# Optimization experiments

Measured on AMD Instinct MI355X. Metric: run time of the kernel, lower is better.

Reference implementation:

```python
import jax, jax.numpy as jnp
import numpy as np

B, T, DIN, H, DOUT = 256, 512, 128, 256, 64
LEAK = 0.01


def setup_inputs() -> dict:
    key = jax.random.key(0)
    k0, k1, k2, k3, k4, k5, k6 = jax.random.split(key, 7)
    inputs = jax.random.normal(k0, (B, T, DIN), dtype=jnp.float32)
    # original uses torch.rand(...) * sqrt(dim) for initial states
    x0 = jax.random.uniform(k1, (B, DOUT), dtype=jnp.float32) * (DOUT ** 0.5)
    h0 = jax.random.uniform(k2, (B, H), dtype=jnp.float32) * (H ** 0.5)
    # nn.Linear default init scale ~ 1/sqrt(fan_in)
    s1 = (DIN + H) ** -0.5
    s2 = H ** -0.5
    W_ih = jax.random.uniform(k3, (H, DIN + H), dtype=jnp.float32, minval=-s1, maxval=s1)
    b_ih = jax.random.uniform(k4, (H,), dtype=jnp.float32, minval=-s1, maxval=s1)
    W_ho = jax.random.uniform(k5, (DOUT, H), dtype=jnp.float32, minval=-s2, maxval=s2)
    b_ho = jax.random.uniform(k6, (DOUT,), dtype=jnp.float32, minval=-s2, maxval=s2)
    return {"inputs": inputs, "x0": x0, "h0": h0,
            "W_ih": W_ih, "b_ih": b_ih, "W_ho": W_ho, "b_ho": b_ho}


def reference(inputs, x0, h0, W_ih, b_ih, W_ho, b_ho):
    # inputs: [B, T, DIN]; scan over time with hidden state resident.
    def step(h, u_t):  # h: [B,H], u_t: [B,DIN]
        comb = jnp.concatenate([u_t, h], axis=1)           # [B, DIN+H]
        pre = comb @ W_ih.T + b_ih                          # [B, H]
        h_new = jnp.where(pre >= 0, pre, LEAK * pre)        # LeakyReLU(0.01)
        x_t = h_new @ W_ho.T + b_ho                         # [B, DOUT]
        return h_new, (x_t, h_new)

    u_seq = jnp.swapaxes(inputs, 0, 1)                      # [T, B, DIN]
    _, (xs, hs) = jax.lax.scan(step, h0, u_seq)
    # prepend initial states -> [B, T+1, *]
    x = jnp.concatenate([x0[:, None, :], jnp.swapaxes(xs, 0, 1)], axis=1)
    h = jnp.concatenate([h0[:, None, :], jnp.swapaxes(hs, 0, 1)], axis=1)
    return x, h
```

## Files before the change

kernel.cpp:

```cpp
#include <hip/hip_runtime.h>

#define BB 256
#define TT 512
#define DIN 128
#define HH 256
#define DOUT 64
#define XROWS ((long)BB * 513)
#define X_ELEMS ((long)BB * 513 * DOUT)

typedef short bf16x8 __attribute__((ext_vector_type(8)));
typedef float f32x4 __attribute__((ext_vector_type(4)));
typedef _Float16 half2_t __attribute__((ext_vector_type(2)));
typedef _Float16 half8_t __attribute__((ext_vector_type(8)));

static __device__ inline short f2bf(float f) {
    unsigned u = __float_as_uint(f);
    unsigned r = (u + 0x7FFFu + ((u >> 16) & 1u)) >> 16;
    return (short)r;
}

static __device__ inline float fdot2f(half2_t a, half2_t b, float c) {
#if __has_builtin(__builtin_amdgcn_fdot2)
    return __builtin_amdgcn_fdot2(a, b, c, false);
#else
    return c + (float)a[0] * (float)b[0] + (float)a[1] * (float)b[1];
#endif
}

__global__ __launch_bounds__(256) void gemm_u(
        const float* __restrict__ inp, const float* __restrict__ W_ih,
        const float* __restrict__ b_ih, float* __restrict__ out_h) {
    __shared__ __align__(16) short lA[64 * 40];
    __shared__ __align__(16) short lB[64 * 40];
    const int tid = threadIdx.x;
    const int wave = tid >> 6, lane = tid & 63;
    const int quad = lane >> 4, l16 = lane & 15;
    const int m0 = blockIdx.x * 64;
    const int n0 = blockIdx.y * 64;
    const int sm = tid >> 2, skg = tid & 3;
    const int sn = tid & 63, bkg = tid >> 6;

    f32x4 acc[4];
#pragma unroll
    for (int i = 0; i < 4; i++) acc[i] = (f32x4){0.f, 0.f, 0.f, 0.f};

#pragma unroll
    for (int k0 = 0; k0 < DIN; k0 += 32) {
        const float4* ap = (const float4*)(inp + (long)(m0 + sm) * DIN + k0 + skg * 8);
        float4 a0 = ap[0], a1 = ap[1];
        const float4* bp = (const float4*)(W_ih + (long)(n0 + sn) * 384 + k0 + bkg * 8);
        float4 b0 = bp[0], b1 = bp[1];
        __syncthreads();
        bf16x8 av, bv;
        av[0] = f2bf(a0.x); av[1] = f2bf(a0.y); av[2] = f2bf(a0.z); av[3] = f2bf(a0.w);
        av[4] = f2bf(a1.x); av[5] = f2bf(a1.y); av[6] = f2bf(a1.z); av[7] = f2bf(a1.w);
        bv[0] = f2bf(b0.x); bv[1] = f2bf(b0.y); bv[2] = f2bf(b0.z); bv[3] = f2bf(b0.w);
        bv[4] = f2bf(b1.x); bv[5] = f2bf(b1.y); bv[6] = f2bf(b1.z); bv[7] = f2bf(b1.w);
        *(bf16x8*)&lA[sm * 40 + skg * 8] = av;
        *(bf16x8*)&lB[sn * 40 + bkg * 8] = bv;
        __syncthreads();
        bf16x8 af = *(const bf16x8*)&lA[(wave * 16 + l16) * 40 + quad * 8];
#pragma unroll
        for (int nt = 0; nt < 4; nt++) {
            bf16x8 bf = *(const bf16x8*)&lB[(nt * 16 + l16) * 40 + quad * 8];
            acc[nt] = __builtin_amdgcn_mfma_f32_16x16x32_bf16(af, bf, acc[nt], 0, 0, 0);
        }
    }
#pragma unroll
    for (int nt = 0; nt < 4; nt++) {
#pragma unroll
        for (int r = 0; r < 4; r++) {
            int m = m0 + wave * 16 + quad * 4 + r;
            int col = n0 + nt * 16 + l16;
            long orow = (long)(m >> 9) * 513 + (m & 511) + 1;
            out_h[orow * HH + col] = acc[nt][r] + b_ih[col];
        }
    }
}

__global__ __launch_bounds__(512) void rnn_seq(
        const float* __restrict__ x0, const float* __restrict__ h0,
        const float* __restrict__ W_ih,
        float* __restrict__ out_x, float* __restrict__ out_h) {
    __shared__ __align__(16) _Float16 hsh[HH];
    __shared__ float part[HH];
    const int b = blockIdx.x;
    const int tid = threadIdx.x;
    const int wave = tid >> 6, lane = tid & 63;
    const int jg = wave & 3, kh = wave >> 2;
    const int j = jg * 64 + lane;
    const int kbase = kh * 128;

    half2_t w[64];
    const float* wr = W_ih + (long)j * 384 + 128 + kbase;
#pragma unroll
    for (int i = 0; i < 32; i++) {
        float4 v = *(const float4*)(wr + 4 * i);
        w[2 * i]     = (half2_t){(_Float16)v.x, (_Float16)v.y};
        w[2 * i + 1] = (half2_t){(_Float16)v.z, (_Float16)v.w};
    }

    float* hrow = out_h + (long)b * 513 * HH;
    if (tid < HH) {
        float hv = h0[(long)b * HH + tid];
        hsh[tid] = (_Float16)hv;
        hrow[tid] = hv;
    }
    if (tid < DOUT) out_x[(long)b * 513 * DOUT + tid] = x0[(long)b * DOUT + tid];
    float c = 0.f;
    if (tid < HH) c = hrow[HH + tid];
    __syncthreads();

    for (int t = 0; t < TT; t++) {
        float a0 = 0.f, a1 = 0.f, a2 = 0.f, a3 = 0.f;
#pragma unroll
        for (int i = 0; i < 16; i++) {
            half8_t hv = *(const half8_t*)&hsh[kbase + 8 * i];
            a0 = fdot2f((half2_t){hv[0], hv[1]}, w[4 * i + 0], a0);
            a1 = fdot2f((half2_t){hv[2], hv[3]}, w[4 * i + 1], a1);
            a2 = fdot2f((half2_t){hv[4], hv[5]}, w[4 * i + 2], a2);
            a3 = fdot2f((half2_t){hv[6], hv[7]}, w[4 * i + 3], a3);
        }
        float s = (a0 + a1) + (a2 + a3);
        if (wave >= 4) part[j] = s;
        __syncthreads();
        if (wave < 4) {
            float tot = s + part[j] + c;
            float hn = tot >= 0.f ? tot : 0.01f * tot;
            hsh[j] = (_Float16)hn;
            hrow[(long)(t + 1) * HH + j] = hn;
            if (t < TT - 1) c = hrow[(long)(t + 2) * HH + j];
        }
        __syncthreads();
    }
}

__global__ __launch_bounds__(256) void gemm_x(
        const float* __restrict__ out_h, const float* __restrict__ W_ho,
        const float* __restrict__ b_ho, float* __restrict__ out_x) {
    __shared__ __align__(16) short lA[64 * 40];
    __shared__ __align__(16) short lB[64 * 40];
    const int tid = threadIdx.x;
    const int wave = tid >> 6, lane = tid & 63;
    const int quad = lane >> 4, l16 = lane & 15;
    const int m0 = blockIdx.x * 64;
    const int bb = m0 >> 9, t0 = m0 & 511;
    const float* hsrc = out_h + ((long)bb * 513 + 1 + t0) * HH;
    float* xdst = out_x + ((long)bb * 513 + 1 + t0) * DOUT;
    const int sm = tid >> 2, skg = tid & 3;
    const int sn = tid & 63, bkg = tid >> 6;

    f32x4 acc[4];
#pragma unroll
    for (int i = 0; i < 4; i++) acc[i] = (f32x4){0.f, 0.f, 0.f, 0.f};

#pragma unroll
    for (int k0 = 0; k0 < HH; k0 += 32) {
        const float4* ap = (const float4*)(hsrc + (long)sm * HH + k0 + skg * 8);
        float4 a0 = ap[0], a1 = ap[1];
        const float4* bp = (const float4*)(W_ho + (long)sn * HH + k0 + bkg * 8);
        float4 b0 = bp[0], b1 = bp[1];
        __syncthreads();
        bf16x8 av, bv;
        av[0] = f2bf(a0.x); av[1] = f2bf(a0.y); av[2] = f2bf(a0.z); av[3] = f2bf(a0.w);
        av[4] = f2bf(a1.x); av[5] = f2bf(a1.y); av[6] = f2bf(a1.z); av[7] = f2bf(a1.w);
        bv[0] = f2bf(b0.x); bv[1] = f2bf(b0.y); bv[2] = f2bf(b0.z); bv[3] = f2bf(b0.w);
        bv[4] = f2bf(b1.x); bv[5] = f2bf(b1.y); bv[6] = f2bf(b1.z); bv[7] = f2bf(b1.w);
        *(bf16x8*)&lA[sm * 40 + skg * 8] = av;
        *(bf16x8*)&lB[sn * 40 + bkg * 8] = bv;
        __syncthreads();
        bf16x8 af = *(const bf16x8*)&lA[(wave * 16 + l16) * 40 + quad * 8];
#pragma unroll
        for (int nt = 0; nt < 4; nt++) {
            bf16x8 bf = *(const bf16x8*)&lB[(nt * 16 + l16) * 40 + quad * 8];
            acc[nt] = __builtin_amdgcn_mfma_f32_16x16x32_bf16(af, bf, acc[nt], 0, 0, 0);
        }
    }
#pragma unroll
    for (int nt = 0; nt < 4; nt++) {
#pragma unroll
        for (int r = 0; r < 4; r++) {
            int mr = wave * 16 + quad * 4 + r;
            int col = nt * 16 + l16;
            xdst[(long)mr * DOUT + col] = acc[nt][r] + b_ho[col];
        }
    }
}

extern "C" void kernel_launch(void* const* d_in, const int* in_sizes, int n_in,
                              void* d_out, int out_size, void* d_ws, size_t ws_size,
                              hipStream_t stream) {
    const float* inp  = (const float*)d_in[0];
    const float* x0   = (const float*)d_in[1];
    const float* h0   = (const float*)d_in[2];
    const float* W_ih = (const float*)d_in[3];
    const float* b_ih = (const float*)d_in[4];
    const float* W_ho = (const float*)d_in[5];
    const float* b_ho = (const float*)d_in[6];
    float* out_x = (float*)d_out;
    float* out_h = out_x + X_ELEMS;

    gemm_u<<<dim3(2048, 4), 256, 0, stream>>>(inp, W_ih, b_ih, out_h);
    rnn_seq<<<dim3(256), 512, 0, stream>>>(x0, h0, W_ih, out_x, out_h);
    gemm_x<<<dim3(2048), 256, 0, stream>>>(out_h, W_ho, b_ho, out_x);
}
```

Measured before the change: 557.7 us.

## Restructure recurrent step with quad DPP reduction, double-buffered state, single barrier

The sequential RNN kernel now uses 256 threads. Each thread computes partial dot products for four hidden units over a quarter of the K range, then combines them across each group of four lanes with DPP butterfly adds instead of a shared-memory partial-sum exchange. The hidden state is double-buffered in LDS, so each timestep needs one barrier instead of two, which shortens the serial critical path. Both GEMM kernels also stage their full K extent into LDS with a single barrier rather than syncing per 32-wide chunk. This raises LDS use and register pressure (128 half2 weights per thread), which may lower occupancy.

```diff
diff --git a/kernel.cpp b/kernel.cpp
--- a/kernel.cpp
+++ b/kernel.cpp
@@ -5,7 +5,6 @@
 #define DIN 128
 #define HH 256
 #define DOUT 64
-#define XROWS ((long)BB * 513)
 #define X_ELEMS ((long)BB * 513 * DOUT)
 
 typedef short bf16x8 __attribute__((ext_vector_type(8)));
@@ -27,11 +26,20 @@
 #endif
 }
 
+static __device__ inline float quad_bfly_add(float x) {
+    int t = __builtin_amdgcn_mov_dpp(__float_as_int(x), 0xB1, 0xF, 0xF, true);
+    x += __int_as_float(t);
+    t = __builtin_amdgcn_mov_dpp(__float_as_int(x), 0x4E, 0xF, 0xF, true);
+    x += __int_as_float(t);
+    return x;
+}
+
+#define SA 136
 __global__ __launch_bounds__(256) void gemm_u(
         const float* __restrict__ inp, const float* __restrict__ W_ih,
         const float* __restrict__ b_ih, float* __restrict__ out_h) {
-    __shared__ __align__(16) short lA[64 * 40];
-    __shared__ __align__(16) short lB[64 * 40];
+    __shared__ __align__(16) short lA[64 * SA];
+    __shared__ __align__(16) short lB[64 * SA];
     const int tid = threadIdx.x;
     const int wave = tid >> 6, lane = tid & 63;
     const int quad = lane >> 4, l16 = lane & 15;
@@ -40,36 +48,44 @@
     const int sm = tid >> 2, skg = tid & 3;
     const int sn = tid & 63, bkg = tid >> 6;
 
+    float4 a4[8], b4[8];
+#pragma unroll
+    for (int c = 0; c < 4; ++c) {
+        const float4* ap = (const float4*)(inp + (long)(m0 + sm) * DIN + c * 32 + skg * 8);
+        a4[2 * c] = ap[0]; a4[2 * c + 1] = ap[1];
+        const float4* bp = (const float4*)(W_ih + (long)(n0 + sn) * 384 + c * 32 + bkg * 8);
+        b4[2 * c] = bp[0]; b4[2 * c + 1] = bp[1];
+    }
+#pragma unroll
+    for (int c = 0; c < 4; ++c) {
+        bf16x8 av, bv;
+        float4 x0 = a4[2 * c], x1 = a4[2 * c + 1];
+        av[0] = f2bf(x0.x); av[1] = f2bf(x0.y); av[2] = f2bf(x0.z); av[3] = f2bf(x0.w);
+        av[4] = f2bf(x1.x); av[5] = f2bf(x1.y); av[6] = f2bf(x1.z); av[7] = f2bf(x1.w);
+        float4 y0 = b4[2 * c], y1 = b4[2 * c + 1];
+        bv[0] = f2bf(y0.x); bv[1] = f2bf(y0.y); bv[2] = f2bf(y0.z); bv[3] = f2bf(y0.w);
+        bv[4] = f2bf(y1.x); bv[5] = f2bf(y1.y); bv[6] = f2bf(y1.z); bv[7] = f2bf(y1.w);
+        *(bf16x8*)&lA[sm * SA + c * 32 + skg * 8] = av;
+        *(bf16x8*)&lB[sn * SA + c * 32 + bkg * 8] = bv;
+    }
+    __syncthreads();
+
     f32x4 acc[4];
 #pragma unroll
     for (int i = 0; i < 4; i++) acc[i] = (f32x4){0.f, 0.f, 0.f, 0.f};
-
-#pragma unroll
-    for (int k0 = 0; k0 < DIN; k0 += 32) {
-        const float4* ap = (const float4*)(inp + (long)(m0 + sm) * DIN + k0 + skg * 8);
-        float4 a0 = ap[0], a1 = ap[1];
-        const float4* bp = (const float4*)(W_ih + (long)(n0 + sn) * 384 + k0 + bkg * 8);
-        float4 b0 = bp[0], b1 = bp[1];
-        __syncthreads();
-        bf16x8 av, bv;
-        av[0] = f2bf(a0.x); av[1] = f2bf(a0.y); av[2] = f2bf(a0.z); av[3] = f2bf(a0.w);
-        av[4] = f2bf(a1.x); av[5] = f2bf(a1.y); av[6] = f2bf(a1.z); av[7] = f2bf(a1.w);
-        bv[0] = f2bf(b0.x); bv[1] = f2bf(b0.y); bv[2] = f2bf(b0.z); bv[3] = f2bf(b0.w);
-        bv[4] = f2bf(b1.x); bv[5] = f2bf(b1.y); bv[6] = f2bf(b1.z); bv[7] = f2bf(b1.w);
-        *(bf16x8*)&lA[sm * 40 + skg * 8] = av;
-        *(bf16x8*)&lB[sn * 40 + bkg * 8] = bv;
-        __syncthreads();
-        bf16x8 af = *(const bf16x8*)&lA[(wave * 16 + l16) * 40 + quad * 8];
-#pragma unroll
-        for (int nt = 0; nt < 4; nt++) {
-            bf16x8 bf = *(const bf16x8*)&lB[(nt * 16 + l16) * 40 + quad * 8];
+#pragma unroll
+    for (int c = 0; c < 4; ++c) {
+        bf16x8 af = *(const bf16x8*)&lA[(wave * 16 + l16) * SA + c * 32 + quad * 8];
+#pragma unroll
+        for (int nt = 0; nt < 4; ++nt) {
+            bf16x8 bf = *(const bf16x8*)&lB[(nt * 16 + l16) * SA + c * 32 + quad * 8];
             acc[nt] = __builtin_amdgcn_mfma_f32_16x16x32_bf16(af, bf, acc[nt], 0, 0, 0);
         }
     }
 #pragma unroll
-    for (int nt = 0; nt < 4; nt++) {
-#pragma unroll
-        for (int r = 0; r < 4; r++) {
+    for (int nt = 0; nt < 4; ++nt) {
+#pragma unroll
+        for (int r = 0; r < 4; ++r) {
             int m = m0 + wave * 16 + quad * 4 + r;
             int col = n0 + nt * 16 + l16;
             long orow = (long)(m >> 9) * 513 + (m & 511) + 1;
@@ -78,68 +94,90 @@
     }
 }
 
-__global__ __launch_bounds__(512) void rnn_seq(
+__global__ __launch_bounds__(256) void rnn_seq(
         const float* __restrict__ x0, const float* __restrict__ h0,
         const float* __restrict__ W_ih,
         float* __restrict__ out_x, float* __restrict__ out_h) {
-    __shared__ __align__(16) _Float16 hsh[HH];
-    __shared__ float part[HH];
+    __shared__ __align__(16) _Float16 hsh[2][4][72];
     const int b = blockIdx.x;
     const int tid = threadIdx.x;
-    const int wave = tid >> 6, lane = tid & 63;
-    const int jg = wave & 3, kh = wave >> 2;
-    const int j = jg * 64 + lane;
-    const int kbase = kh * 128;
-
-    half2_t w[64];
-    const float* wr = W_ih + (long)j * 384 + 128 + kbase;
-#pragma unroll
-    for (int i = 0; i < 32; i++) {
-        float4 v = *(const float4*)(wr + 4 * i);
-        w[2 * i]     = (half2_t){(_Float16)v.x, (_Float16)v.y};
-        w[2 * i + 1] = (half2_t){(_Float16)v.z, (_Float16)v.w};
+    const int g = tid >> 2;
+    const int q = tid & 3;
+    const int jm = (g << 2) + q;
+
+    half2_t w[4][32];
+    {
+        const float* base = W_ih + 128 + 64 * q;
+#pragma unroll
+        for (int jp = 0; jp < 4; ++jp) {
+            const float* wr = base + (long)(4 * g + jp) * 384;
+#pragma unroll
+            for (int i = 0; i < 16; ++i) {
+                float4 v = *(const float4*)(wr + 4 * i);
+                w[jp][2 * i]     = (half2_t){(_Float16)v.x, (_Float16)v.y};
+                w[jp][2 * i + 1] = (half2_t){(_Float16)v.z, (_Float16)v.w};
+            }
+        }
     }
 
     float* hrow = out_h + (long)b * 513 * HH;
-    if (tid < HH) {
-        float hv = h0[(long)b * HH + tid];
-        hsh[tid] = (_Float16)hv;
-        hrow[tid] = hv;
+    {
+        float hv = h0[(long)b * HH + jm];
+        hrow[jm] = hv;
+        hsh[0][jm >> 6][jm & 63] = (_Float16)hv;
     }
     if (tid < DOUT) out_x[(long)b * 513 * DOUT + tid] = x0[(long)b * DOUT + tid];
-    float c = 0.f;
-    if (tid < HH) c = hrow[HH + tid];
+    float u = hrow[HH + jm];
     __syncthreads();
 
-    for (int t = 0; t < TT; t++) {
+    int cur = 0;
+    for (int t = 0; t < TT; ++t) {
+        const _Float16* hs = &hsh[cur][q][0];
         float a0 = 0.f, a1 = 0.f, a2 = 0.f, a3 = 0.f;
 #pragma unroll
-        for (int i = 0; i < 16; i++) {
-            half8_t hv = *(const half8_t*)&hsh[kbase + 8 * i];
-            a0 = fdot2f((half2_t){hv[0], hv[1]}, w[4 * i + 0], a0);
-            a1 = fdot2f((half2_t){hv[2], hv[3]}, w[4 * i + 1], a1);
-            a2 = fdot2f((half2_t){hv[4], hv[5]}, w[4 * i + 2], a2);
-            a3 = fdot2f((half2_t){hv[6], hv[7]}, w[4 * i + 3], a3);
-        }
-        float s = (a0 + a1) + (a2 + a3);
-        if (wave >= 4) part[j] = s;
+        for (int c = 0; c < 8; ++c) {
+            half8_t hv = *(const half8_t*)(hs + 8 * c);
+            half2_t p0 = {hv[0], hv[1]}, p1 = {hv[2], hv[3]};
+            half2_t p2 = {hv[4], hv[5]}, p3 = {hv[6], hv[7]};
+            a0 = fdot2f(p0, w[0][4 * c + 0], a0);
+            a0 = fdot2f(p1, w[0][4 * c + 1], a0);
+            a0 = fdot2f(p2, w[0][4 * c + 2], a0);
+            a0 = fdot2f(p3, w[0][4 * c + 3], a0);
+            a1 = fdot2f(p0, w[1][4 * c + 0], a1);
+            a1 = fdot2f(p1, w[1][4 * c + 1], a1);
+            a1 = fdot2f(p2, w[1][4 * c + 2], a1);
+            a1 = fdot2f(p3, w[1][4 * c + 3], a1);
+            a2 = fdot2f(p0, w[2][4 * c + 0], a2);
+            a2 = fdot2f(p1, w[2][4 * c + 1], a2);
+            a2 = fdot2f(p2, w[2][4 * c + 2], a2);
+            a2 = fdot2f(p3, w[2][4 * c + 3], a2);
+            a3 = fdot2f(p0, w[3][4 * c + 0], a3);
+            a3 = fdot2f(p1, w[3][4 * c + 1], a3);
+            a3 = fdot2f(p2, w[3][4 * c + 2], a3);
+            a3 = fdot2f(p3, w[3][4 * c + 3], a3);
+        }
+        a0 = quad_bfly_add(a0);
+        a1 = quad_bfly_add(a1);
+        a2 = quad_bfly_add(a2);
+        a3 = quad_bfly_add(a3);
+        float s = (q == 0) ? a0 : (q == 1) ? a1 : (q == 2) ? a2 : a3;
+        float tot = s + u;
+        float hn = tot >= 0.f ? tot : 0.01f * tot;
+        int nxt = cur ^ 1;
+        hsh[nxt][jm >> 6][jm & 63] = (_Float16)hn;
+        hrow[(long)(t + 1) * HH + jm] = hn;
+        if (t < TT - 1) u = hrow[(long)(t + 2) * HH + jm];
         __syncthreads();
-        if (wave < 4) {
-            float tot = s + part[j] + c;
-            float hn = tot >= 0.f ? tot : 0.01f * tot;
-            hsh[j] = (_Float16)hn;
-            hrow[(long)(t + 1) * HH + j] = hn;
-            if (t < TT - 1) c = hrow[(long)(t + 2) * HH + j];
-        }
-        __syncthreads();
-    }
-}
-
+        cur = nxt;
+    }
+}
+
+#define SX 264
 __global__ __launch_bounds__(256) void gemm_x(
         const float* __restrict__ out_h, const float* __restrict__ W_ho,
         const float* __restrict__ b_ho, float* __restrict__ out_x) {
-    __shared__ __align__(16) short lA[64 * 40];
-    __shared__ __align__(16) short lB[64 * 40];
+    __shared__ __align__(16) short lA[64 * SX];
+    __shared__ __align__(16) short lB[64 * SX];
     const int tid = threadIdx.x;
     const int wave = tid >> 6, lane = tid & 63;
     const int quad = lane >> 4, l16 = lane & 15;
@@ -150,36 +188,49 @@
     const int sm = tid >> 2, skg = tid & 3;
     const int sn = tid & 63, bkg = tid >> 6;
 
+#pragma unroll
+    for (int ph = 0; ph < 2; ++ph) {
+        float4 a4[8], b4[8];
+#pragma unroll
+        for (int c = 0; c < 4; ++c) {
+            int k0 = ph * 128 + c * 32;
+            const float4* ap = (const float4*)(hsrc + (long)sm * HH + k0 + skg * 8);
+            a4[2 * c] = ap[0]; a4[2 * c + 1] = ap[1];
+            const float4* bp = (const float4*)(W_ho + (long)sn * HH + k0 + bkg * 8);
+            b4[2 * c] = bp[0]; b4[2 * c + 1] = bp[1];
+        }
+#pragma unroll
+        for (int c = 0; c < 4; ++c) {
+            int k0 = ph * 128 + c * 32;
+            bf16x8 av, bv;
+            float4 x0 = a4[2 * c], x1 = a4[2 * c + 1];
+            av[0] = f2bf(x0.x); av[1] = f2bf(x0.y); av[2] = f2bf(x0.z); av[3] = f2bf(x0.w);
+            av[4] = f2bf(x1.x); av[5] = f2bf(x1.y); av[6] = f2bf(x1.z); av[7] = f2bf(x1.w);
+            float4 y0 = b4[2 * c], y1 = b4[2 * c + 1];
+            bv[0] = f2bf(y0.x); bv[1] = f2bf(y0.y); bv[2] = f2bf(y0.z); bv[3] = f2bf(y0.w);
+            bv[4] = f2bf(y1.x); bv[5] = f2bf(y1.y); bv[6] = f2bf(y1.z); bv[7] = f2bf(y1.w);
+            *(bf16x8*)&lA[sm * SX + k0 + skg * 8] = av;
+            *(bf16x8*)&lB[sn * SX + k0 + bkg * 8] = bv;
+        }
+    }
+    __syncthreads();
+
     f32x4 acc[4];
 #pragma unroll
     for (int i = 0; i < 4; i++) acc[i] = (f32x4){0.f, 0.f, 0.f, 0.f};
-
-#pragma unroll
-    for (int k0 = 0; k0 < HH; k0 += 32) {
-        const float4* ap = (const float4*)(hsrc + (long)sm * HH + k0 + skg * 8);
-        float4 a0 = ap[0], a1 = ap[1];
-        const float4* bp = (const float4*)(W_ho + (long)sn * HH + k0 + bkg * 8);
-        float4 b0 = bp[0], b1 = bp[1];
-        __syncthreads();
-        bf16x8 av, bv;
-        av[0] = f2bf(a0.x); av[1] = f2bf(a0.y); av[2] = f2bf(a0.z); av[3] = f2bf(a0.w);
-        av[4] = f2bf(a1.x); av[5] = f2bf(a1.y); av[6] = f2bf(a1.z); av[7] = f2bf(a1.w);
-        bv[0] = f2bf(b0.x); bv[1] = f2bf(b0.y); bv[2] = f2bf(b0.z); bv[3] = f2bf(b0.w);
-        bv[4] = f2bf(b1.x); bv[5] = f2bf(b1.y); bv[6] = f2bf(b1.z); bv[7] = f2bf(b1.w);
-        *(bf16x8*)&lA[sm * 40 + skg * 8] = av;
-        *(bf16x8*)&lB[sn * 40 + bkg * 8] = bv;
-        __syncthreads();
-        bf16x8 af = *(const bf16x8*)&lA[(wave * 16 + l16) * 40 + quad * 8];
-#pragma unroll
-        for (int nt = 0; nt < 4; nt++) {
-            bf16x8 bf = *(const bf16x8*)&lB[(nt * 16 + l16) * 40 + quad * 8];
+#pragma unroll
+    for (int c = 0; c < 8; ++c) {
+        bf16x8 af = *(const bf16x8*)&lA[(wave * 16 + l16) * SX + c * 32 + quad * 8];
+#pragma unroll
+        for (int nt = 0; nt < 4; ++nt) {
+            bf16x8 bf = *(const bf16x8*)&lB[(nt * 16 + l16) * SX + c * 32 + quad * 8];
             acc[nt] = __builtin_amdgcn_mfma_f32_16x16x32_bf16(af, bf, acc[nt], 0, 0, 0);
         }
     }
 #pragma unroll
-    for (int nt = 0; nt < 4; nt++) {
-#pragma unroll
-        for (int r = 0; r < 4; r++) {
+    for (int nt = 0; nt < 4; ++nt) {
+#pragma unroll
+        for (int r = 0; r < 4; ++r) {
             int mr = wave * 16 + quad * 4 + r;
             int col = nt * 16 + l16;
             xdst[(long)mr * DOUT + col] = acc[nt][r] + b_ho[col];
@@ -201,6 +252,6 @@
     float* out_h = out_x + X_ELEMS;
 
     gemm_u<<<dim3(2048, 4), 256, 0, stream>>>(inp, W_ih, b_ih, out_h);
-    rnn_seq<<<dim3(256), 512, 0, stream>>>(x0, h0, W_ih, out_x, out_h);
+    rnn_seq<<<dim3(256), 256, 0, stream>>>(x0, h0, W_ih, out_x, out_h);
     gemm_x<<<dim3(2048), 256, 0, stream>>>(out_h, W_ho, b_ho, out_x);
 }
```

New measurement: 516.2 us. 7.4% less time.
